# Kernel optimization log

Hardware: AMD Instinct MI355X
Metric: run time of the kernel (lower is better)

The kernel has to match this reference:

```python
import jax, jax.numpy as jnp
import numpy as np

B, C, H, S, DC = 32768, 1024, 1024, 8, 64  # batch, num_classes, hidden_dim, num_styles, calibrator dim

def setup_inputs() -> dict:
    key = jax.random.key(0)
    ks = jax.random.split(key, 12)
    inp = {
        "logits": jax.random.normal(ks[0], (B, C), dtype=jnp.float32),
        "style_idx": jax.random.randint(ks[1], (B,), 0, S, dtype=jnp.int32),
        # learned params
        "style_emb": jax.random.normal(ks[2], (S, H), dtype=jnp.float32),
        "Wa1": jax.random.normal(ks[3], (C + H, H), dtype=jnp.float32) * (1.0 / np.sqrt(C + H)),
        "ba1": jnp.zeros((H,), dtype=jnp.float32),
        "Wa2": jax.random.normal(ks[4], (H, C), dtype=jnp.float32) * (1.0 / np.sqrt(H)),
        "ba2": jnp.zeros((C,), dtype=jnp.float32),
        # per-style confidence calibrators: Linear(C,64) -> ReLU -> Linear(64,1) -> Sigmoid
        "Wc1": jax.random.normal(ks[5], (S, C, DC), dtype=jnp.float32) * (1.0 / np.sqrt(C)),
        "bc1": jnp.zeros((S, DC), dtype=jnp.float32),
        "Wc2": jax.random.normal(ks[6], (S, DC), dtype=jnp.float32) * (1.0 / np.sqrt(DC)),
        "bc2": jnp.zeros((S,), dtype=jnp.float32),
    }
    return inp

def reference(logits, style_idx, style_emb, Wa1, ba1, Wa2, ba2, Wc1, bc1, Wc2, bc2):
    # style embedding lookup + adapter MLP (residual on logits)
    emb = style_emb[style_idx]                                  # (B, H)
    combined = jnp.concatenate([logits, emb], axis=1)           # (B, C+H)
    hidden = jax.nn.relu(combined @ Wa1 + ba1)                  # (B, H)
    adjusted_logits = logits + hidden @ Wa2 + ba2               # (B, C)
    probs = jax.nn.softmax(adjusted_logits, axis=1)             # (B, C)
    # expert-routed confidence calibration: compute all styles densely, select per sample
    h = jax.nn.relu(jnp.einsum('bc,scd->bsd', probs, Wc1) + bc1)   # (B, S, DC)
    conf_all = jax.nn.sigmoid(jnp.einsum('bsd,sd->bs', h, Wc2) + bc2)  # (B, S)
    calibrated_confidence = jnp.take_along_axis(conf_all, style_idx[:, None].astype(jnp.int32), axis=1)  # (B, 1)
    return adjusted_logits, calibrated_confidence
```

## Files before the change

kernel.cpp:

```cpp
#include <hip/hip_runtime.h>
#include <hip/hip_bf16.h>
#include <stdint.h>

typedef __hip_bfloat16 bf16;
typedef __attribute__((ext_vector_type(8))) short short8;
typedef __attribute__((ext_vector_type(4))) float f32x4;

#define NB 32768
#define NC 1024
#define NH 1024
#define NS 8
#define NDC 64

__device__ __forceinline__ void gload_lds16(const void* g, void* l) {
    __builtin_amdgcn_global_load_lds((const __attribute__((address_space(1))) void*)g,
                                     (__attribute__((address_space(3))) void*)l, 16, 0, 0);
}

__device__ __forceinline__ short f2bf(float x) {
    bf16 h = __float2bfloat16(x);
    short s;
    __builtin_memcpy(&s, &h, 2);
    return s;
}

__global__ __launch_bounds__(256) void convert_kernel(
    const float* __restrict__ in, bf16* __restrict__ out)
{
    const size_t i = ((size_t)blockIdx.x * 256 + threadIdx.x) * 8;
    float4 a = *(const float4*)(in + i);
    float4 b = *(const float4*)(in + i + 4);
    short8 v;
    v[0] = f2bf(a.x); v[1] = f2bf(a.y); v[2] = f2bf(a.z); v[3] = f2bf(a.w);
    v[4] = f2bf(b.x); v[5] = f2bf(b.y); v[6] = f2bf(b.z); v[7] = f2bf(b.w);
    *(short8*)((short*)out + i) = v;
}

__global__ __launch_bounds__(256) void transpose_kernel(
    const float* __restrict__ in, bf16* __restrict__ out,
    int R, int Ccols, long long in_bs, long long out_bs)
{
    __shared__ float tile[32][33];
    const float* inb = in + (long long)blockIdx.z * in_bs;
    bf16* outb = out + (long long)blockIdx.z * out_bs;
    int c0 = blockIdx.x * 32, r0 = blockIdx.y * 32;
    int tx = threadIdx.x, ty = threadIdx.y;
#pragma unroll
    for (int i = 0; i < 32; i += 8)
        tile[ty + i][tx] = inb[(size_t)(r0 + ty + i) * Ccols + c0 + tx];
    __syncthreads();
#pragma unroll
    for (int i = 0; i < 32; i += 8)
        outb[(size_t)(c0 + ty + i) * R + r0 + tx] = __float2bfloat16(tile[tx][ty + i]);
}

__global__ __launch_bounds__(256) void style_partial_kernel(
    const float* __restrict__ style_emb, const float* __restrict__ Wa1,
    float* __restrict__ partial)
{
    const int h = (blockIdx.x & 3) * 256 + threadIdx.x;
    const int ks = blockIdx.x >> 2;
    float acc[NS];
#pragma unroll
    for (int s = 0; s < NS; ++s) acc[s] = 0.f;
#pragma unroll
    for (int kk = 0; kk < 16; ++kk) {
        const int k = ks * 16 + kk;
        const float w = Wa1[(size_t)(NC + k) * NH + h];
#pragma unroll
        for (int s = 0; s < NS; ++s)
            acc[s] += style_emb[s * NH + k] * w;
    }
#pragma unroll
    for (int s = 0; s < NS; ++s)
        partial[((size_t)ks * NS + s) * NH + h] = acc[s];
}

__global__ __launch_bounds__(256) void style_reduce_kernel(
    const float* __restrict__ partial, const float* __restrict__ ba1,
    float* __restrict__ out)
{
    const int i = blockIdx.x * 256 + threadIdx.x;
    const int h = i & (NH - 1);
    const int s = i >> 10;
    float acc = ba1[h];
#pragma unroll 8
    for (int ks = 0; ks < 64; ++ks)
        acc += partial[((size_t)ks * NS + s) * NH + h];
    out[i] = acc;
}

template<int MODE>
__global__ __launch_bounds__(256, 2) void gemm_kernel(
    const bf16* __restrict__ A, const bf16* __restrict__ BT,
    bf16* __restrict__ Cb, float* __restrict__ Cf,
    int N, int K,
    const float* __restrict__ style_contrib, const int* __restrict__ style_idx,
    const float* __restrict__ resid, const float* __restrict__ bias)
{
    __shared__ short lA[128 * 32];
    __shared__ short lB[128 * 32];

    const int t = threadIdx.x;
    const int lane = t & 63;
    const int wave = t >> 6;
    const int wr = wave >> 1;
    const int wc = wave & 1;
    const int bm0 = blockIdx.y * 128;
    const int bn0 = blockIdx.x * 128;

    const int r0 = t >> 2;
    const int c8 = (t & 3) * 8;

    const int mrow = lane & 15;
    const int quad = lane >> 4;

    f32x4 acc[4][4];
#pragma unroll
    for (int i = 0; i < 4; ++i)
#pragma unroll
        for (int j = 0; j < 4; ++j) acc[i][j] = (f32x4){0.f, 0.f, 0.f, 0.f};

    const bf16* gA = A + (size_t)(bm0 + r0) * K + c8;
    const bf16* gB = BT + (size_t)(bn0 + r0) * K + c8;

    for (int k0 = 0; k0 < K; k0 += 32) {
        gload_lds16(gA + k0, lA + t * 8);
        gload_lds16(gA + (size_t)64 * K + k0, lA + 2048 + t * 8);
        gload_lds16(gB + k0, lB + t * 8);
        gload_lds16(gB + (size_t)64 * K + k0, lB + 2048 + t * 8);
        __syncthreads();

        short8 af[4], bfr[4];
#pragma unroll
        for (int i = 0; i < 4; ++i)
            af[i] = *(const short8*)(lA + (wr * 64 + i * 16 + mrow) * 32 + quad * 8);
#pragma unroll
        for (int j = 0; j < 4; ++j)
            bfr[j] = *(const short8*)(lB + (wc * 64 + j * 16 + mrow) * 32 + quad * 8);
#pragma unroll
        for (int i = 0; i < 4; ++i)
#pragma unroll
            for (int j = 0; j < 4; ++j)
                acc[i][j] = __builtin_amdgcn_mfma_f32_16x16x32_bf16(af[i], bfr[j], acc[i][j], 0, 0, 0);
        __syncthreads();
    }

#pragma unroll
    for (int i = 0; i < 4; ++i) {
#pragma unroll
        for (int r = 0; r < 4; ++r) {
            const int grow = bm0 + wr * 64 + i * 16 + quad * 4 + r;
            const float* scrow = nullptr;
            const float* resrow = nullptr;
            if (MODE == 0) scrow = style_contrib + (size_t)style_idx[grow] * N;
            if (MODE == 1) resrow = resid + (size_t)grow * N;
#pragma unroll
            for (int j = 0; j < 4; ++j) {
                const int gcol = bn0 + wc * 64 + j * 16 + mrow;
                float v = acc[i][j][r];
                if (MODE == 0) {
                    v += scrow[gcol];
                    v = fmaxf(v, 0.f);
                    Cb[(size_t)grow * N + gcol] = __float2bfloat16(v);
                } else if (MODE == 1) {
                    v += resrow[gcol] + bias[gcol];
                    Cf[(size_t)grow * N + gcol] = v;
                } else {
                    v += bias[gcol];
                    v = fmaxf(v, 0.f);
                    Cb[(size_t)grow * N + gcol] = __float2bfloat16(v);
                }
            }
        }
    }
}

__global__ __launch_bounds__(256) void softmax_kernel(
    const float* __restrict__ in, bf16* __restrict__ out)
{
    const size_t row = blockIdx.x;
    const float* x = in + row * NC;
    bf16* o = out + row * NC;
    const int t = threadIdx.x;
    __shared__ float red[8];

    float v[4];
    float m = -1e30f;
#pragma unroll
    for (int i = 0; i < 4; ++i) {
        v[i] = x[t + i * 256];
        m = fmaxf(m, v[i]);
    }
#pragma unroll
    for (int off = 1; off < 64; off <<= 1) m = fmaxf(m, __shfl_xor(m, off, 64));
    const int wv = t >> 6;
    if ((t & 63) == 0) red[wv] = m;
    __syncthreads();
    const float gm = fmaxf(fmaxf(red[0], red[1]), fmaxf(red[2], red[3]));

    float s = 0.f;
#pragma unroll
    for (int i = 0; i < 4; ++i) {
        v[i] = __expf(v[i] - gm);
        s += v[i];
    }
#pragma unroll
    for (int off = 1; off < 64; off <<= 1) s += __shfl_xor(s, off, 64);
    if ((t & 63) == 0) red[4 + wv] = s;
    __syncthreads();
    const float inv = 1.0f / (red[4] + red[5] + red[6] + red[7]);
#pragma unroll
    for (int i = 0; i < 4; ++i) o[t + i * 256] = __float2bfloat16(v[i] * inv);
}

__global__ __launch_bounds__(256) void conf_kernel(
    const bf16* __restrict__ hcal, const int* __restrict__ style_idx,
    const float* __restrict__ Wc2, const float* __restrict__ bc2,
    float* __restrict__ out)
{
    const int t = threadIdx.x;
    const int lane = t & 63;
    const int b = blockIdx.x * 4 + (t >> 6);
    const int s = style_idx[b];
    float p = __bfloat162float(hcal[(size_t)b * (NS * NDC) + s * NDC + lane]) *
              Wc2[s * NDC + lane];
#pragma unroll
    for (int off = 1; off < 64; off <<= 1) p += __shfl_xor(p, off, 64);
    if (lane == 0) {
        float z = p + bc2[s];
        out[b] = 1.0f / (1.0f + __expf(-z));
    }
}

extern "C" void kernel_launch(void* const* d_in, const int* in_sizes, int n_in,
                              void* d_out, int out_size, void* d_ws, size_t ws_size,
                              hipStream_t stream) {
    const float* logits    = (const float*)d_in[0];
    const int*   style_idx = (const int*)d_in[1];
    const float* style_emb = (const float*)d_in[2];
    const float* Wa1       = (const float*)d_in[3];
    const float* ba1       = (const float*)d_in[4];
    const float* Wa2       = (const float*)d_in[5];
    const float* ba2       = (const float*)d_in[6];
    const float* Wc1       = (const float*)d_in[7];
    const float* bc1       = (const float*)d_in[8];
    const float* Wc2       = (const float*)d_in[9];
    const float* bc2       = (const float*)d_in[10];

    char* ws = (char*)d_ws;
    bf16* logits_b = (bf16*)ws;        ws += (size_t)NB * NC * 2;
    bf16* hidden = (bf16*)ws;          ws += (size_t)NB * NH * 2;
    bf16* W1T = (bf16*)ws;             ws += (size_t)NC * NH * 2;
    bf16* W2T = (bf16*)ws;             ws += (size_t)NH * NC * 2;
    bf16* Wc1T = (bf16*)ws;            ws += (size_t)NS * NDC * NC * 2;
    float* style_contrib = (float*)ws; ws += (size_t)NS * NH * 4;
    float* style_partial = (float*)ws; ws += (size_t)64 * NS * NH * 4;
    bf16* hcal = logits_b;

    float* adjusted = (float*)d_out;
    float* conf_out = (float*)d_out + (size_t)NB * NC;

    convert_kernel<<<(NB * NC) / (256 * 8), 256, 0, stream>>>(logits, logits_b);

    dim3 tb(32, 8);
    transpose_kernel<<<dim3(32, 32, 1), tb, 0, stream>>>(Wa1, W1T, NC, NH, 0, 0);
    transpose_kernel<<<dim3(32, 32, 1), tb, 0, stream>>>(Wa2, W2T, NH, NC, 0, 0);
    transpose_kernel<<<dim3(2, 32, NS), tb, 0, stream>>>(Wc1, Wc1T, NC, NDC,
                                                         (long long)NC * NDC, (long long)NDC * NC);
    style_partial_kernel<<<256, 256, 0, stream>>>(style_emb, Wa1, style_partial);
    style_reduce_kernel<<<NS * NH / 256, 256, 0, stream>>>(style_partial, ba1, style_contrib);

    gemm_kernel<0><<<dim3(NH / 128, NB / 128), 256, 0, stream>>>(
        logits_b, W1T, hidden, nullptr, NH, NC, style_contrib, style_idx, nullptr, nullptr);
    gemm_kernel<1><<<dim3(NC / 128, NB / 128), 256, 0, stream>>>(
        hidden, W2T, nullptr, adjusted, NC, NH, nullptr, nullptr, logits, ba2);
    softmax_kernel<<<NB, 256, 0, stream>>>(adjusted, hidden);
    gemm_kernel<2><<<dim3((NS * NDC) / 128, NB / 128), 256, 0, stream>>>(
        hidden, Wc1T, hcal, nullptr, NS * NDC, NC, nullptr, nullptr, nullptr, bc1);
    conf_kernel<<<NB / 4, 256, 0, stream>>>(hcal, style_idx, Wc2, bc2, conf_out);
}
```

Measured before the change: 570.0 us.

## Route calibrator GEMM by style with sorted gather, fuse conf epilogue; swizzle GEMM tiles

Computes only the calibrator for each sample's own style instead of all eight styles. A histogram, a plan and a scatter pass sort batch indices by style, and a new gathered GEMM over 128-row groups fuses bias, ReLU, the Wc2 dot product and the sigmoid into its epilogue. This removes the dense 512-wide GEMM and the intermediate hcal write and read. Separately, the main GEMMs remap block indices in an 8-way interleaved swizzle to improve L2 locality. It adds several small serial kernels, including a single-thread plan kernel and atomics, and the calibrator GEMM launches only 264 blocks, which may leave the GPU underused.

```diff
diff --git a/kernel.cpp b/kernel.cpp
--- a/kernel.cpp
+++ b/kernel.cpp
@@ -11,6 +11,7 @@
 #define NH 1024
 #define NS 8
 #define NDC 64
+#define MAXBLK 264
 
 __device__ __forceinline__ void gload_lds16(const void* g, void* l) {
     __builtin_amdgcn_global_load_lds((const __attribute__((address_space(1))) void*)g,
@@ -106,8 +107,13 @@
     const int wave = t >> 6;
     const int wr = wave >> 1;
     const int wc = wave & 1;
-    const int bm0 = blockIdx.y * 128;
-    const int bn0 = blockIdx.x * 128;
+
+    const int nwg = gridDim.x * gridDim.y;
+    const int flat = blockIdx.y * gridDim.x + blockIdx.x;
+    const int cpx = nwg >> 3;
+    const int swz = (flat & 7) * cpx + (flat >> 3);
+    const int bm0 = (swz / gridDim.x) * 128;
+    const int bn0 = (swz % gridDim.x) * 128;
 
     const int r0 = t >> 2;
     const int c8 = (t & 3) * 8;
@@ -163,13 +169,9 @@
                     v += scrow[gcol];
                     v = fmaxf(v, 0.f);
                     Cb[(size_t)grow * N + gcol] = __float2bfloat16(v);
-                } else if (MODE == 1) {
+                } else {
                     v += resrow[gcol] + bias[gcol];
                     Cf[(size_t)grow * N + gcol] = v;
-                } else {
-                    v += bias[gcol];
-                    v = fmaxf(v, 0.f);
-                    Cb[(size_t)grow * N + gcol] = __float2bfloat16(v);
                 }
             }
         }
@@ -214,22 +216,141 @@
     for (int i = 0; i < 4; ++i) o[t + i * 256] = __float2bfloat16(v[i] * inv);
 }
 
-__global__ __launch_bounds__(256) void conf_kernel(
-    const bf16* __restrict__ hcal, const int* __restrict__ style_idx,
-    const float* __restrict__ Wc2, const float* __restrict__ bc2,
-    float* __restrict__ out)
-{
+
+__global__ __launch_bounds__(256) void hist_kernel(
+    const int* __restrict__ idx, int* __restrict__ cnt)
+{
+    __shared__ int h[NS];
+    if (threadIdx.x < NS) h[threadIdx.x] = 0;
+    __syncthreads();
+    atomicAdd(&h[idx[blockIdx.x * 256 + threadIdx.x]], 1);
+    __syncthreads();
+    if (threadIdx.x < NS) atomicAdd(&cnt[threadIdx.x], h[threadIdx.x]);
+}
+
+__global__ void plan_kernel(const int* __restrict__ cnt, int* __restrict__ cursor,
+                            int* __restrict__ blk_style, int* __restrict__ blk_seg0,
+                            int* __restrict__ blk_nv)
+{
+    if (threadIdx.x != 0 || blockIdx.x != 0) return;
+    int base = 0, nb = 0;
+    for (int s = 0; s < NS; ++s) {
+        cursor[s] = base;
+        const int c = cnt[s];
+        for (int i = 0; i < c; i += 128) {
+            blk_style[nb] = s;
+            blk_seg0[nb] = base + i;
+            blk_nv[nb] = min(128, c - i);
+            ++nb;
+        }
+        base += c;
+    }
+    for (int b = nb; b < MAXBLK; ++b) { blk_style[b] = 0; blk_seg0[b] = 0; blk_nv[b] = 0; }
+}
+
+__global__ __launch_bounds__(256) void scatter_kernel(
+    const int* __restrict__ idx, int* __restrict__ cursor, int* __restrict__ order)
+{
+    const int b = blockIdx.x * 256 + threadIdx.x;
+    const int s = idx[b];
+    const int lane = threadIdx.x & 63;
+    int pos = 0;
+#pragma unroll 1
+    for (int ss = 0; ss < NS; ++ss) {
+        const unsigned long long m = __ballot(s == ss);
+        if (m == 0ull) continue;
+        const int leader = __ffsll(m) - 1;
+        int base = 0;
+        if (lane == leader) base = atomicAdd(&cursor[ss], __popcll(m));
+        base = __shfl(base, leader, 64);
+        if (s == ss)
+            pos = base + __popcll(m & ((1ull << lane) - 1ull));
+    }
+    order[pos] = b;
+}
+
+__global__ __launch_bounds__(256, 2) void gemm_cal_kernel(
+    const bf16* __restrict__ probs, const bf16* __restrict__ Wc1T,
+    const int* __restrict__ order, const int* __restrict__ blk_style,
+    const int* __restrict__ blk_seg0, const int* __restrict__ blk_nv,
+    const float* __restrict__ bc1, const float* __restrict__ Wc2,
+    const float* __restrict__ bc2, float* __restrict__ conf_out)
+{
+    const int nv = blk_nv[blockIdx.x];
+    if (nv == 0) return;
+    const int s = blk_style[blockIdx.x];
+    const int seg0 = blk_seg0[blockIdx.x];
+
+    __shared__ short lA[128 * 32];
+    __shared__ short lB[64 * 32];
+    __shared__ int rid[128];
+
     const int t = threadIdx.x;
     const int lane = t & 63;
-    const int b = blockIdx.x * 4 + (t >> 6);
-    const int s = style_idx[b];
-    float p = __bfloat162float(hcal[(size_t)b * (NS * NDC) + s * NDC + lane]) *
-              Wc2[s * NDC + lane];
-#pragma unroll
-    for (int off = 1; off < 64; off <<= 1) p += __shfl_xor(p, off, 64);
-    if (lane == 0) {
-        float z = p + bc2[s];
-        out[b] = 1.0f / (1.0f + __expf(-z));
+    const int wave = t >> 6;
+
+    if (t < 128) rid[t] = order[seg0 + min(t, nv - 1)];
+    __syncthreads();
+
+    const int r0 = t >> 2, c8 = (t & 3) * 8;
+    const bf16* gA0 = probs + (size_t)rid[r0] * NC + c8;
+    const bf16* gA1 = probs + (size_t)rid[64 + r0] * NC + c8;
+    const bf16* gB  = Wc1T + ((size_t)s * NDC + r0) * NC + c8;
+
+    const int mrow = lane & 15;
+    const int quad = lane >> 4;
+
+    f32x4 acc[2][4];
+#pragma unroll
+    for (int i = 0; i < 2; ++i)
+#pragma unroll
+        for (int j = 0; j < 4; ++j) acc[i][j] = (f32x4){0.f, 0.f, 0.f, 0.f};
+
+    for (int k0 = 0; k0 < NC; k0 += 32) {
+        gload_lds16(gA0 + k0, lA + t * 8);
+        gload_lds16(gA1 + k0, lA + 2048 + t * 8);
+        gload_lds16(gB + k0, lB + t * 8);
+        __syncthreads();
+
+        short8 af[2], bfr[4];
+#pragma unroll
+        for (int i = 0; i < 2; ++i)
+            af[i] = *(const short8*)(lA + (wave * 32 + i * 16 + mrow) * 32 + quad * 8);
+#pragma unroll
+        for (int j = 0; j < 4; ++j)
+            bfr[j] = *(const short8*)(lB + (j * 16 + mrow) * 32 + quad * 8);
+#pragma unroll
+        for (int i = 0; i < 2; ++i)
+#pragma unroll
+            for (int j = 0; j < 4; ++j)
+                acc[i][j] = __builtin_amdgcn_mfma_f32_16x16x32_bf16(af[i], bfr[j], acc[i][j], 0, 0, 0);
+        __syncthreads();
+    }
+
+    float bcv[4], wcv[4];
+#pragma unroll
+    for (int j = 0; j < 4; ++j) {
+        const int d = j * 16 + mrow;
+        bcv[j] = bc1[s * NDC + d];
+        wcv[j] = Wc2[s * NDC + d];
+    }
+    const float bias2 = bc2[s];
+#pragma unroll
+    for (int i = 0; i < 2; ++i) {
+#pragma unroll
+        for (int r = 0; r < 4; ++r) {
+            float p = 0.f;
+#pragma unroll
+            for (int j = 0; j < 4; ++j) {
+                const float v = acc[i][j][r] + bcv[j];
+                p += fmaxf(v, 0.f) * wcv[j];
+            }
+#pragma unroll
+            for (int off = 1; off < 16; off <<= 1) p += __shfl_xor(p, off, 64);
+            const int lrow = wave * 32 + i * 16 + quad * 4 + r;
+            if (mrow == 0 && lrow < nv)
+                conf_out[rid[lrow]] = 1.0f / (1.0f + __expf(-(p + bias2)));
+        }
     }
 }
 
@@ -256,10 +377,20 @@
     bf16* Wc1T = (bf16*)ws;            ws += (size_t)NS * NDC * NC * 2;
     float* style_contrib = (float*)ws; ws += (size_t)NS * NH * 4;
     float* style_partial = (float*)ws; ws += (size_t)64 * NS * NH * 4;
-    bf16* hcal = logits_b;
+    int* sty_cnt   = (int*)ws;         ws += 64;
+    int* cursor    = (int*)ws;         ws += 64;
+    int* order     = (int*)ws;         ws += (size_t)NB * 4;
+    int* blk_style = (int*)ws;         ws += MAXBLK * 4;
+    int* blk_seg0  = (int*)ws;         ws += MAXBLK * 4;
+    int* blk_nv    = (int*)ws;         ws += MAXBLK * 4;
 
     float* adjusted = (float*)d_out;
     float* conf_out = (float*)d_out + (size_t)NB * NC;
+
+    hipMemsetAsync(sty_cnt, 0, 64, stream);
+    hist_kernel<<<NB / 256, 256, 0, stream>>>(style_idx, sty_cnt);
+    plan_kernel<<<1, 64, 0, stream>>>(sty_cnt, cursor, blk_style, blk_seg0, blk_nv);
+    scatter_kernel<<<NB / 256, 256, 0, stream>>>(style_idx, cursor, order);
 
     convert_kernel<<<(NB * NC) / (256 * 8), 256, 0, stream>>>(logits, logits_b);
 
@@ -276,7 +407,6 @@
     gemm_kernel<1><<<dim3(NC / 128, NB / 128), 256, 0, stream>>>(
         hidden, W2T, nullptr, adjusted, NC, NH, nullptr, nullptr, logits, ba2);
     softmax_kernel<<<NB, 256, 0, stream>>>(adjusted, hidden);
-    gemm_kernel<2><<<dim3((NS * NDC) / 128, NB / 128), 256, 0, stream>>>(
-        hidden, Wc1T, hcal, nullptr, NS * NDC, NC, nullptr, nullptr, nullptr, bc1);
-    conf_kernel<<<NB / 4, 256, 0, stream>>>(hcal, style_idx, Wc2, bc2, conf_out);
-}
+    gemm_cal_kernel<<<MAXBLK, 256, 0, stream>>>(hidden, Wc1T, order, blk_style, blk_seg0,
+                                                blk_nv, bc1, Wc2, bc2, conf_out);
+}
```

New measurement: 575.9 us. Within noise of the previous version (+1.0%).

## Fuse calibrator epilogue into GEMM and swizzle workgroup order across XCDs

Applied to the files above, without the earlier changes.

Replaces the calibrator GEMM plus separate confidence kernel with one GEMM whose epilogue applies bias, ReLU, the Wc2 dot product and a cross-lane reduction, then writes the sigmoid only for the matching style. This removes the bf16 hcal round trip through memory and one kernel launch. It also remaps workgroup IDs with an 8-way XCD swizzle in all GEMMs to improve L2 locality on the multi-die GPU. The fused path still computes all eight styles densely, and the swizzle assumes the workgroup count divides by 8.

```diff
diff --git a/kernel.cpp b/kernel.cpp
--- a/kernel.cpp
+++ b/kernel.cpp
@@ -106,8 +106,13 @@
     const int wave = t >> 6;
     const int wr = wave >> 1;
     const int wc = wave & 1;
-    const int bm0 = blockIdx.y * 128;
-    const int bn0 = blockIdx.x * 128;
+
+    const int nwg = gridDim.x * gridDim.y;
+    const int flat = blockIdx.y * gridDim.x + blockIdx.x;
+    const int cpx = nwg >> 3;
+    const int swz = (flat & 7) * cpx + (flat >> 3);
+    const int bm0 = (swz / gridDim.x) * 128;
+    const int bn0 = (swz % gridDim.x) * 128;
 
     const int r0 = t >> 2;
     const int c8 = (t & 3) * 8;
@@ -163,15 +168,98 @@
                     v += scrow[gcol];
                     v = fmaxf(v, 0.f);
                     Cb[(size_t)grow * N + gcol] = __float2bfloat16(v);
-                } else if (MODE == 1) {
+                } else {
                     v += resrow[gcol] + bias[gcol];
                     Cf[(size_t)grow * N + gcol] = v;
-                } else {
-                    v += bias[gcol];
-                    v = fmaxf(v, 0.f);
-                    Cb[(size_t)grow * N + gcol] = __float2bfloat16(v);
                 }
             }
+        }
+    }
+}
+
+__global__ __launch_bounds__(256, 2) void gemm_conf_kernel(
+    const bf16* __restrict__ A, const bf16* __restrict__ BT,
+    int N, int K,
+    const int* __restrict__ style_idx,
+    const float* __restrict__ bc1, const float* __restrict__ Wc2,
+    const float* __restrict__ bc2, float* __restrict__ conf_out)
+{
+    __shared__ short lA[128 * 32];
+    __shared__ short lB[128 * 32];
+
+    const int t = threadIdx.x;
+    const int lane = t & 63;
+    const int wave = t >> 6;
+    const int wr = wave >> 1;
+    const int wc = wave & 1;
+
+    const int nwg = gridDim.x * gridDim.y;
+    const int flat = blockIdx.y * gridDim.x + blockIdx.x;
+    const int cpx = nwg >> 3;
+    const int swz = (flat & 7) * cpx + (flat >> 3);
+    const int bm0 = (swz / gridDim.x) * 128;
+    const int bn0 = (swz % gridDim.x) * 128;
+
+    const int r0 = t >> 2;
+    const int c8 = (t & 3) * 8;
+
+    const int mrow = lane & 15;
+    const int quad = lane >> 4;
+
+    f32x4 acc[4][4];
+#pragma unroll
+    for (int i = 0; i < 4; ++i)
+#pragma unroll
+        for (int j = 0; j < 4; ++j) acc[i][j] = (f32x4){0.f, 0.f, 0.f, 0.f};
+
+    const bf16* gA = A + (size_t)(bm0 + r0) * K + c8;
+    const bf16* gB = BT + (size_t)(bn0 + r0) * K + c8;
+
+    for (int k0 = 0; k0 < K; k0 += 32) {
+        gload_lds16(gA + k0, lA + t * 8);
+        gload_lds16(gA + (size_t)64 * K + k0, lA + 2048 + t * 8);
+        gload_lds16(gB + k0, lB + t * 8);
+        gload_lds16(gB + (size_t)64 * K + k0, lB + 2048 + t * 8);
+        __syncthreads();
+
+        short8 af[4], bfr[4];
+#pragma unroll
+        for (int i = 0; i < 4; ++i)
+            af[i] = *(const short8*)(lA + (wr * 64 + i * 16 + mrow) * 32 + quad * 8);
+#pragma unroll
+        for (int j = 0; j < 4; ++j)
+            bfr[j] = *(const short8*)(lB + (wc * 64 + j * 16 + mrow) * 32 + quad * 8);
+#pragma unroll
+        for (int i = 0; i < 4; ++i)
+#pragma unroll
+            for (int j = 0; j < 4; ++j)
+                acc[i][j] = __builtin_amdgcn_mfma_f32_16x16x32_bf16(af[i], bfr[j], acc[i][j], 0, 0, 0);
+        __syncthreads();
+    }
+
+    const int s_w = (bn0 >> 6) + wc;
+    float bcv[4], wcv[4];
+#pragma unroll
+    for (int j = 0; j < 4; ++j) {
+        const int d = j * 16 + mrow;
+        bcv[j] = bc1[s_w * NDC + d];
+        wcv[j] = Wc2[s_w * NDC + d];
+    }
+    const float bias2 = bc2[s_w];
+
+#pragma unroll
+    for (int i = 0; i < 4; ++i) {
+#pragma unroll
+        for (int r = 0; r < 4; ++r) {
+            const int grow = bm0 + wr * 64 + i * 16 + quad * 4 + r;
+            float p = 0.f;
+#pragma unroll
+            for (int j = 0; j < 4; ++j)
+                p += fmaxf(acc[i][j][r] + bcv[j], 0.f) * wcv[j];
+#pragma unroll
+            for (int off = 1; off < 16; off <<= 1) p += __shfl_xor(p, off, 64);
+            if (mrow == 0 && style_idx[grow] == s_w)
+                conf_out[grow] = 1.0f / (1.0f + __expf(-(p + bias2)));
         }
     }
 }
@@ -212,25 +300,6 @@
     const float inv = 1.0f / (red[4] + red[5] + red[6] + red[7]);
 #pragma unroll
     for (int i = 0; i < 4; ++i) o[t + i * 256] = __float2bfloat16(v[i] * inv);
-}
-
-__global__ __launch_bounds__(256) void conf_kernel(
-    const bf16* __restrict__ hcal, const int* __restrict__ style_idx,
-    const float* __restrict__ Wc2, const float* __restrict__ bc2,
-    float* __restrict__ out)
-{
-    const int t = threadIdx.x;
-    const int lane = t & 63;
-    const int b = blockIdx.x * 4 + (t >> 6);
-    const int s = style_idx[b];
-    float p = __bfloat162float(hcal[(size_t)b * (NS * NDC) + s * NDC + lane]) *
-              Wc2[s * NDC + lane];
-#pragma unroll
-    for (int off = 1; off < 64; off <<= 1) p += __shfl_xor(p, off, 64);
-    if (lane == 0) {
-        float z = p + bc2[s];
-        out[b] = 1.0f / (1.0f + __expf(-z));
-    }
 }
 
 extern "C" void kernel_launch(void* const* d_in, const int* in_sizes, int n_in,
@@ -256,7 +325,6 @@
     bf16* Wc1T = (bf16*)ws;            ws += (size_t)NS * NDC * NC * 2;
     float* style_contrib = (float*)ws; ws += (size_t)NS * NH * 4;
     float* style_partial = (float*)ws; ws += (size_t)64 * NS * NH * 4;
-    bf16* hcal = logits_b;
 
     float* adjusted = (float*)d_out;
     float* conf_out = (float*)d_out + (size_t)NB * NC;
@@ -276,7 +344,6 @@
     gemm_kernel<1><<<dim3(NC / 128, NB / 128), 256, 0, stream>>>(
         hidden, W2T, nullptr, adjusted, NC, NH, nullptr, nullptr, logits, ba2);
     softmax_kernel<<<NB, 256, 0, stream>>>(adjusted, hidden);
-    gemm_kernel<2><<<dim3((NS * NDC) / 128, NB / 128), 256, 0, stream>>>(
-        hidden, Wc1T, hcal, nullptr, NS * NDC, NC, nullptr, nullptr, nullptr, bc1);
-    conf_kernel<<<NB / 4, 256, 0, stream>>>(hcal, style_idx, Wc2, bc2, conf_out);
-}
+    gemm_conf_kernel<<<dim3((NS * NDC) / 128, NB / 128), 256, 0, stream>>>(
+        hidden, Wc1T, NS * NDC, NC, style_idx, bc1, Wc2, bc2, conf_out);
+}
```

Result: faster. 528.0 us (-7.4%).
